# Performance work log

Hardware: AMD Instinct MI355X
Metric: run time of the kernel (lower is better)

## Reference

```python
import jax, jax.numpy as jnp
import numpy as np

THRESHOLD = 0.5
NEG_POS = 3
ALPHA = 1.0


def cxcy_to_xy(c):
    return jnp.concatenate([c[..., :2] - c[..., 2:] / 2, c[..., :2] + c[..., 2:] / 2], axis=-1)


def xy_to_cxcy(x):
    return jnp.concatenate([(x[..., :2] + x[..., 2:]) / 2, x[..., 2:] - x[..., :2]], axis=-1)


def encode_gcxgcy(cxcy, priors_cxcy):
    # SSD offset encoding with variances (10, 10, 5, 5)
    return jnp.concatenate([
        (cxcy[..., :2] - priors_cxcy[..., :2]) / (priors_cxcy[..., 2:] / 10.0),
        jnp.log(cxcy[..., 2:] / priors_cxcy[..., 2:]) * 5.0,
    ], axis=-1)


def compute_iou(a, b):
    # a: [n,4] xyxy, b: [m,4] xyxy -> [n,m]
    lt = jnp.maximum(a[:, None, :2], b[None, :, :2])
    rb = jnp.minimum(a[:, None, 2:], b[None, :, 2:])
    wh = jnp.clip(rb - lt, 0.0)
    inter = wh[..., 0] * wh[..., 1]
    area_a = (a[:, 2] - a[:, 0]) * (a[:, 3] - a[:, 1])
    area_b = (b[:, 2] - b[:, 0]) * (b[:, 3] - b[:, 1])
    return inter / (area_a[:, None] + area_b[None, :] - inter)


def _match_one(boxes, labels, db_xy, db_cxcy):
    # boxes: [n_obj,4] xyxy, labels: [n_obj], priors: [P,4]
    n_obj = boxes.shape[0]
    overlaps = compute_iou(boxes, db_xy)                 # [n_obj, P]
    ov_per_box = jnp.max(overlaps, axis=0)               # [P]
    obj_per_box = jnp.argmax(overlaps, axis=0)           # [P]
    box_per_obj = jnp.argmax(overlaps, axis=1)           # [n_obj]
    # force each gt to own its best prior
    obj_per_box = obj_per_box.at[box_per_obj].set(jnp.arange(n_obj))
    ov_per_box = ov_per_box.at[box_per_obj].set(1.0)
    lbl = labels[obj_per_box]                            # [P]
    lbl = jnp.where(ov_per_box < THRESHOLD, 0, lbl)      # background below threshold
    true_locs = encode_gcxgcy(xy_to_cxcy(boxes[obj_per_box]), db_cxcy)  # [P,4]
    return true_locs, lbl


def smooth_l1(x):
    ax = jnp.abs(x)
    return jnp.where(ax < 1.0, 0.5 * x * x, ax - 0.5)


def reference(loc_pred, cls_pred, gt_boxes, gt_labels, default_boxes):
    # loc_pred: [B,P,4], cls_pred: [B,P,C], gt_boxes: [B,n_obj,4],
    # gt_labels: [B,n_obj] int, default_boxes: [P,4] cxcywh
    db_xy = cxcy_to_xy(default_boxes)
    true_locs, true_labels = jax.vmap(_match_one, in_axes=(0, 0, None, None))(
        gt_boxes, gt_labels, db_xy, default_boxes)      # [B,P,4], [B,P]

    positive = true_labels > 0                           # [B,P]
    n_pos = jnp.sum(positive, axis=1)                    # [B]
    n_pos_total = jnp.sum(n_pos).astype(loc_pred.dtype)

    # localization loss: SmoothL1 mean over positive box elements
    loc_elem = smooth_l1(loc_pred - true_locs)           # [B,P,4]
    loc_loss = jnp.sum(loc_elem * positive[..., None]) / (n_pos_total * 4.0)

    # confidence loss: cross entropy with 3:1 hard negative mining
    logp = jax.nn.log_softmax(cls_pred, axis=-1)         # [B,P,C]
    ce = -jnp.take_along_axis(logp, true_labels[..., None], axis=-1)[..., 0]  # [B,P]
    conf_pos = jnp.sum(ce * positive)
    ce_neg = jnp.where(positive, 0.0, ce)
    # rank negatives by loss (descending) per image; take top neg_pos * n_pos
    ranks = jnp.argsort(jnp.argsort(-ce_neg, axis=1), axis=1)  # [B,P]
    hard_neg = ranks < (NEG_POS * n_pos)[:, None]
    conf_hard = jnp.sum(ce_neg * hard_neg)
    conf_loss = (conf_pos + conf_hard) / n_pos_total

    return conf_loss + ALPHA * loc_loss


def setup_inputs() -> dict:
    key = jax.random.key(0)
    ks = jax.random.split(key, 8)
    B, P, C, n_obj = 64, 8732, 81, 32

    # priors in cxcywh, valid in [0,1]
    db_cxy = jax.random.uniform(ks[0], (P, 2), minval=0.05, maxval=0.95)
    db_wh = jax.random.uniform(ks[1], (P, 2), minval=0.05, maxval=0.3)
    default_boxes = jnp.concatenate([db_cxy, db_wh], axis=-1).astype(jnp.float32)

    # gt boxes: valid xyxy built from centers and sizes
    g_cxy = jax.random.uniform(ks[2], (B, n_obj, 2), minval=0.2, maxval=0.8)
    g_wh = jax.random.uniform(ks[3], (B, n_obj, 2), minval=0.1, maxval=0.4)
    gt_boxes = jnp.concatenate([g_cxy - g_wh / 2, g_cxy + g_wh / 2], axis=-1).astype(jnp.float32)
    gt_labels = jax.random.randint(ks[4], (B, n_obj), 1, C)

    loc_pred = jax.random.normal(ks[5], (B, P, 4), dtype=jnp.float32) * 0.1
    cls_pred = jax.random.normal(ks[6], (B, P, C), dtype=jnp.float32)

    return {"loc_pred": loc_pred, "cls_pred": cls_pred, "gt_boxes": gt_boxes,
            "gt_labels": gt_labels, "default_boxes": default_boxes}
```

## Files before the change

### kernel.cpp

```cpp
#include <hip/hip_runtime.h>
#include <hip/hip_bf16.h>
#include <math.h>

#define BB 64
#define PP 8732
#define CC 81
#define NOBJ 32
#define CHUNKS ((PP + 255) / 256)
#define NPRI (BB * PP)
#define WTILE 16
#define WTW (WTILE * CC)
#define NWT (NPRI / WTILE)
#define CE_BLOCKS 1792
#define TPW 5

typedef float f4 __attribute__((ext_vector_type(4)));

__device__ __forceinline__ float sl1(float x) {
    float ax = fabsf(x);
    return (ax < 1.0f) ? 0.5f * x * x : ax - 0.5f;
}

__global__ __launch_bounds__(256) void k_bestprior(
    const float* __restrict__ gt_boxes,
    const float* __restrict__ dbox,
    int*   __restrict__ bp,
    float* __restrict__ acc,
    int*   __restrict__ npt,
    int*   __restrict__ done,
    int*   __restrict__ n_pos)
{
    __shared__ float s_bv[4];
    __shared__ int   s_bi[4];
    const int tid = threadIdx.x, lane = tid & 63, wave = tid >> 6;
    const int b = blockIdx.x >> 5;
    const int o = blockIdx.x & 31;

    if (blockIdx.x == 0) {
        if (tid < BB) n_pos[tid] = 0;
        else if (tid < BB + 3) acc[tid - BB] = 0.0f;
        else if (tid == BB + 3) *npt = 0;
        else if (tid == BB + 4) *done = 0;
    }

    const float* g = gt_boxes + (b * NOBJ + o) * 4;
    float gx0 = g[0], gy0 = g[1], gx1 = g[2], gy1 = g[3];
    float garea = (gx1 - gx0) * (gy1 - gy0);

    float best = -1.0f; int bpp = 0x7fffffff;
    for (int p = tid; p < PP; p += 256) {
        float4 db = reinterpret_cast<const float4*>(dbox)[p];
        float px0 = db.x - db.z * 0.5f, py0 = db.y - db.w * 0.5f;
        float px1 = db.x + db.z * 0.5f, py1 = db.y + db.w * 0.5f;
        float parea = db.z * db.w;
        float lx = fmaxf(px0, gx0), ly = fmaxf(py0, gy0);
        float rx = fminf(px1, gx1), ry = fminf(py1, gy1);
        float w = fmaxf(rx - lx, 0.0f), h = fmaxf(ry - ly, 0.0f);
        float inter = w * h;
        float iou = inter / (garea + parea - inter);
        if (iou > best) { best = iou; bpp = p; }
    }
#pragma unroll
    for (int m = 32; m > 0; m >>= 1) {
        float ov = __shfl_xor(best, m);
        int   op = __shfl_xor(bpp, m);
        if (ov > best || (ov == best && op < bpp)) { best = ov; bpp = op; }
    }
    if (lane == 0) { s_bv[wave] = best; s_bi[wave] = bpp; }
    __syncthreads();
    if (tid == 0) {
        for (int w2 = 1; w2 < 4; ++w2) {
            if (s_bv[w2] > best || (s_bv[w2] == best && s_bi[w2] < bpp)) {
                best = s_bv[w2]; bpp = s_bi[w2];
            }
        }
        bp[b * NOBJ + o] = bpp;
    }
}

__global__ __launch_bounds__(256) void k_assign(
    const float* __restrict__ loc_pred,
    const float* __restrict__ gt_boxes,
    const int*   __restrict__ gt_labels,
    const float* __restrict__ dbox,
    const int*   __restrict__ bp,
    int*   __restrict__ true_label,
    int*   __restrict__ n_pos,
    float* __restrict__ acc,
    int*   __restrict__ n_pos_total)
{
    __shared__ float s_gx0[NOBJ], s_gy0[NOBJ], s_gx1[NOBJ], s_gy1[NOBJ], s_garea[NOBJ];
    __shared__ float s_gcx[NOBJ], s_gcy[NOBJ], s_gw[NOBJ], s_gh[NOBJ];
    __shared__ int   s_glbl[NOBJ], s_bp[NOBJ];
    __shared__ float red_f[256];
    __shared__ int   red_i[256];

    const int b     = blockIdx.x / CHUNKS;
    const int chunk = blockIdx.x % CHUNKS;
    const int tid   = threadIdx.x;
    const int p     = chunk * 256 + tid;

    if (tid < NOBJ) {
        float x0 = gt_boxes[(b * NOBJ + tid) * 4 + 0];
        float y0 = gt_boxes[(b * NOBJ + tid) * 4 + 1];
        float x1 = gt_boxes[(b * NOBJ + tid) * 4 + 2];
        float y1 = gt_boxes[(b * NOBJ + tid) * 4 + 3];
        s_gx0[tid] = x0; s_gy0[tid] = y0; s_gx1[tid] = x1; s_gy1[tid] = y1;
        s_garea[tid] = (x1 - x0) * (y1 - y0);
        s_gcx[tid] = (x0 + x1) * 0.5f;
        s_gcy[tid] = (y0 + y1) * 0.5f;
        s_gw[tid]  = x1 - x0;
        s_gh[tid]  = y1 - y0;
        s_glbl[tid] = gt_labels[b * NOBJ + tid];
        s_bp[tid]   = bp[b * NOBJ + tid];
    }
    __syncthreads();

    float loc_local = 0.0f;
    int   np_local  = 0;

    if (p < PP) {
        float4 db = reinterpret_cast<const float4*>(dbox)[p];
        float px0 = db.x - db.z * 0.5f, py0 = db.y - db.w * 0.5f;
        float px1 = db.x + db.z * 0.5f, py1 = db.y + db.w * 0.5f;
        float parea = db.z * db.w;

        float best = -1.0f; int bo = 0;
#pragma unroll
        for (int o = 0; o < NOBJ; ++o) {
            float lx = fmaxf(px0, s_gx0[o]), ly = fmaxf(py0, s_gy0[o]);
            float rx = fminf(px1, s_gx1[o]), ry = fminf(py1, s_gy1[o]);
            float w = fmaxf(rx - lx, 0.0f), h = fmaxf(ry - ly, 0.0f);
            float inter = w * h;
            float iou = inter / (s_garea[o] + parea - inter);
            if (iou > best) { best = iou; bo = o; }
        }
        int forced = -1;
#pragma unroll
        for (int o = 0; o < NOBJ; ++o)
            if (s_bp[o] == p) forced = o;

        int o_use, lbl;
        if (forced >= 0) { o_use = forced; lbl = s_glbl[forced]; }
        else             { o_use = bo; lbl = (best < 0.5f) ? 0 : s_glbl[bo]; }

        true_label[b * PP + p] = lbl;
        if (lbl > 0) {
            np_local = 1;
            float g0 = (s_gcx[o_use] - db.x) / (db.z / 10.0f);
            float g1 = (s_gcy[o_use] - db.y) / (db.w / 10.0f);
            float g2 = logf(s_gw[o_use] / db.z) * 5.0f;
            float g3 = logf(s_gh[o_use] / db.w) * 5.0f;
            float4 lp = reinterpret_cast<const float4*>(loc_pred)[b * PP + p];
            loc_local = sl1(lp.x - g0) + sl1(lp.y - g1) + sl1(lp.z - g2) + sl1(lp.w - g3);
        }
    }

    red_f[tid] = loc_local;
    red_i[tid] = np_local;
    __syncthreads();
#pragma unroll
    for (int st = 128; st > 0; st >>= 1) {
        if (tid < st) { red_f[tid] += red_f[tid + st]; red_i[tid] += red_i[tid + st]; }
        __syncthreads();
    }
    if (tid == 0) {
        if (red_f[0] != 0.0f) atomicAdd(&acc[0], red_f[0]);
        if (red_i[0]) {
            atomicAdd(&n_pos[b], red_i[0]);
            atomicAdd(n_pos_total, red_i[0]);
        }
    }
}

__global__ __launch_bounds__(256) void k_ce(
    const float* __restrict__ cls_pred,
    const int*   __restrict__ true_label,
    float* __restrict__ ce_neg,
    float* __restrict__ acc)
{
    __shared__ float s_x[4][WTW];
    __shared__ float s_red[4];
    const int tid  = threadIdx.x;
    const int wave = tid >> 6, lane = tid & 63;
    const int rloc = lane >> 2, q = lane & 3;

    float* sx = s_x[wave];
    f4* dst = reinterpret_cast<f4*>(sx);
    const f4* tile4 = reinterpret_cast<const f4*>(sx);

    const int seg_start = rloc * CC + q * 20;
    const int seg_len   = (q == 3) ? 21 : 20;
    const int ws        = seg_start >> 2;
    const int a         = seg_start & 3;
    const int hi_cnt    = a + seg_len - 20;

    const float L2E = 1.4426950408889634f;
    const float LN2 = 0.6931471805599453f;
    float local = 0.0f;

    const int g    = blockIdx.x * 4 + wave;
    int wt         = g * TPW;
    const int wend = (wt + TPW < NWT) ? wt + TPW : NWT;

    f4 r0, r1, r2, r3, r4, r5;
    int lbl_next = 0;
    if (wt < wend) {
        const f4* src = reinterpret_cast<const f4*>(cls_pred + (size_t)wt * WTW);
        r0 = src[lane];
        r1 = src[64 + lane];
        r2 = src[128 + lane];
        r3 = src[192 + lane];
        r4 = src[256 + lane];
        if (lane < 4) r5 = src[320 + lane];
        lbl_next = true_label[wt * WTILE + rloc];
    }

    while (wt < wend) {
        dst[lane] = r0; dst[64 + lane] = r1; dst[128 + lane] = r2;
        dst[192 + lane] = r3; dst[256 + lane] = r4;
        if (lane < 4) dst[320 + lane] = r5;
        const int lbl  = lbl_next;
        const int pidx = wt * WTILE + rloc;

        const int wtn = wt + 1;
        if (wtn < wend) {
            const f4* src = reinterpret_cast<const f4*>(cls_pred + (size_t)wtn * WTW);
            r0 = src[lane];
            r1 = src[64 + lane];
            r2 = src[128 + lane];
            r3 = src[192 + lane];
            r4 = src[256 + lane];
            if (lane < 4) r5 = src[320 + lane];
            lbl_next = true_label[wtn * WTILE + rloc];
        }

        f4 w0 = tile4[ws];
        f4 w1 = tile4[ws + 1];
        f4 w2 = tile4[ws + 2];
        f4 w3 = tile4[ws + 3];
        f4 w4 = tile4[ws + 4];
        f4 w5 = tile4[ws + 5];

        float s0 = 0.0f, s1 = 0.0f;
#pragma unroll
        for (int k = 0; k < 4; ++k) {
            float e = exp2f(w0[k] * L2E);
            s0 += (k >= a) ? e : 0.0f;
        }
#pragma unroll
        for (int k = 0; k < 4; ++k) s1 += exp2f(w1[k] * L2E);
#pragma unroll
        for (int k = 0; k < 4; ++k) s0 += exp2f(w2[k] * L2E);
#pragma unroll
        for (int k = 0; k < 4; ++k) s1 += exp2f(w3[k] * L2E);
#pragma unroll
        for (int k = 0; k < 4; ++k) s0 += exp2f(w4[k] * L2E);
#pragma unroll
        for (int k = 0; k < 4; ++k) {
            float e = exp2f(w5[k] * L2E);
            s1 += (k < hi_cnt) ? e : 0.0f;
        }
        float s = s0 + s1;
        s += __shfl_xor(s, 1);
        s += __shfl_xor(s, 2);

        if (q == 0) {
            float ce = fmaf(log2f(s), LN2, -sx[rloc * CC + lbl]);
            ce_neg[pidx] = (lbl > 0) ? 0.0f : ce;
            local += (lbl > 0) ? ce : 0.0f;
        }
        wt = wtn;
    }

#pragma unroll
    for (int m = 32; m > 0; m >>= 1) local += __shfl_xor(local, m);
    if (lane == 0) s_red[wave] = local;
    __syncthreads();
    if (tid == 0) {
        float tot = s_red[0] + s_red[1] + s_red[2] + s_red[3];
        if (tot != 0.0f) atomicAdd(&acc[1], tot);
    }
}

__global__ __launch_bounds__(1024) void k_select(
    const float* __restrict__ ce_neg,
    const int*   __restrict__ n_pos,
    float* __restrict__ acc,
    const int*  __restrict__ n_pos_total,
    int*   __restrict__ done,
    float* __restrict__ out)
{
    __shared__ unsigned int sv[PP];
    __shared__ unsigned int h16[16][256];
    __shared__ unsigned int hist[257];
    __shared__ unsigned int wtot[4];
    __shared__ unsigned int s_prefix, s_krem;
    __shared__ float rf[16];
    __shared__ int   ri[16];

    const int b = blockIdx.x, tid = threadIdx.x;
    const int lane = tid & 63, w = tid >> 6;

    int K = n_pos[b] * 3;
    if (K > PP) K = PP;

    if (K > 0) {
        for (int i = tid; i < PP; i += 1024)
            sv[i] = __float_as_uint(ce_neg[b * PP + i]);

        unsigned int prefix = 0, krem = (unsigned int)K;
        for (int shift = 24; shift >= 0; shift -= 8) {
            unsigned int* hflat = &h16[0][0];
            for (int j = tid; j < 16 * 256; j += 1024) hflat[j] = 0;
            if (tid == 0) hist[256] = 0;
            __syncthreads();
            unsigned int mask_hi = (shift == 24) ? 0u : (0xFFFFFFFFu << (shift + 8));
            for (int i = tid; i < PP; i += 1024) {
                unsigned int v = sv[i];
                if ((v & mask_hi) == prefix)
                    atomicAdd(&h16[w][(v >> shift) & 0xFFu], 1u);
            }
            __syncthreads();
            unsigned int s = 0;
            if (tid < 256) {
#pragma unroll
                for (int r = 0; r < 16; ++r) s += h16[r][tid];
#pragma unroll
                for (int off = 1; off < 64; off <<= 1) {
                    unsigned int aa = __shfl_down(s, off);
                    if (lane + off < 64) s += aa;
                }
                if (lane == 0) wtot[w] = s;
            }
            __syncthreads();
            if (tid < 256) {
                unsigned int sb = 0;
#pragma unroll
                for (int r = 0; r < 16; ++r) sb += h16[r][tid];
                unsigned int suf = sb;
#pragma unroll
                for (int off = 1; off < 64; off <<= 1) {
                    unsigned int aa = __shfl_down(suf, off);
                    if (lane + off < 64) suf += aa;
                }
                for (int w2 = w + 1; w2 < 4; ++w2) suf += wtot[w2];
                hist[tid] = suf;
            }
            __syncthreads();
            if (tid < 256) {
                unsigned int suf  = hist[tid];
                unsigned int suf1 = hist[tid + 1];
                if (suf >= krem && suf1 < krem) {
                    s_prefix = prefix | ((unsigned int)tid << shift);
                    s_krem   = krem - suf1;
                }
            }
            __syncthreads();
            prefix = s_prefix; krem = s_krem;
        }
        float cutoff = __uint_as_float(prefix);

        float sum_gt = 0.0f; int cnt_gt = 0;
        for (int i = tid; i < PP; i += 1024) {
            float v = __uint_as_float(sv[i]);
            if (v > cutoff) { sum_gt += v; cnt_gt++; }
        }
#pragma unroll
        for (int m = 32; m > 0; m >>= 1) {
            sum_gt += __shfl_xor(sum_gt, m);
            cnt_gt += __shfl_xor(cnt_gt, m);
        }
        if (lane == 0) { rf[w] = sum_gt; ri[w] = cnt_gt; }
        __syncthreads();
        if (tid == 0) {
            float sg = 0.0f; int cg = 0;
#pragma unroll
            for (int r = 0; r < 16; ++r) { sg += rf[r]; cg += ri[r]; }
            atomicAdd(&acc[2], sg + (float)(K - cg) * cutoff);
        }
    }

    if (tid == 0) {
        __threadfence();
        int old = atomicAdd(done, 1);
        if (old == BB - 1) {
            float a0 = atomicAdd(&acc[0], 0.0f);
            float a1 = atomicAdd(&acc[1], 0.0f);
            float a2 = atomicAdd(&acc[2], 0.0f);
            float npt = (float)atomicAdd((int*)n_pos_total, 0);
            out[0] = (a1 + a2) / npt + a0 / (npt * 4.0f);
        }
    }
}

extern "C" void kernel_launch(void* const* d_in, const int* in_sizes, int n_in,
                              void* d_out, int out_size, void* d_ws, size_t ws_size,
                              hipStream_t stream) {
    const float* loc_pred  = (const float*)d_in[0];
    const float* cls_pred  = (const float*)d_in[1];
    const float* gt_boxes  = (const float*)d_in[2];
    const int*   gt_labels = (const int*)d_in[3];
    const float* dbox      = (const float*)d_in[4];
    float* out = (float*)d_out;

    float* acc        = (float*)d_ws;
    int*   npt        = (int*)d_ws + 3;
    int*   done       = (int*)d_ws + 4;
    int*   n_pos      = (int*)d_ws + 8;
    int*   bp         = (int*)d_ws + 8 + BB;
    int*   true_label = (int*)d_ws + 8 + BB + BB * NOBJ;
    float* ce_neg     = (float*)(true_label + (size_t)NPRI);

    k_bestprior<<<BB * NOBJ, 256, 0, stream>>>(gt_boxes, dbox, bp,
                                               acc, npt, done, n_pos);
    k_assign<<<BB * CHUNKS, 256, 0, stream>>>(loc_pred, gt_boxes, gt_labels, dbox, bp,
                                              true_label, n_pos, acc, npt);
    k_ce<<<CE_BLOCKS, 256, 0, stream>>>(cls_pred, true_label, ce_neg, acc);
    k_select<<<BB, 1024, 0, stream>>>(ce_neg, n_pos, acc, npt, done, out);
}
```

Measured before the change: 151.6 us.

## Stream CE logit tiles directly into LDS with double-buffered global_load_lds

The cross-entropy kernel now copies each 16-prior logit tile straight from global memory into LDS with global_load_lds, instead of staging it through registers and then writing it to LDS. Each wave double-buffers its tiles and uses explicit vmcnt waits to overlap the next tile's load with the current tile's reduction. All labels are prefetched up front. Blocks shrink to two waves and the grid grows to keep the same work split. The aim is to cut VGPR pressure and LDS store instructions on the bandwidth-bound logit stream, at the cost of hand-managed waitcnts that depend on how the compiler counts loads.

Result: slower. 169.8 us (+12.0%).

```diff
diff --git a/kernel.cpp b/kernel.cpp
--- a/kernel.cpp
+++ b/kernel.cpp
@@ -11,10 +11,12 @@
 #define WTILE 16
 #define WTW (WTILE * CC)
 #define NWT (NPRI / WTILE)
-#define CE_BLOCKS 1792
 #define TPW 5
+#define CE_BLOCKS 3493
 
 typedef float f4 __attribute__((ext_vector_type(4)));
+typedef const __attribute__((address_space(1))) void g_void;
+typedef __attribute__((address_space(3))) void l_void;
 
 __device__ __forceinline__ float sl1(float x) {
     float ax = fabsf(x);
@@ -173,21 +175,42 @@
     }
 }
 
-__global__ __launch_bounds__(256) void k_ce(
+#define ISSUE6(WT, LBASE)                                                         \
+    {                                                                             \
+        const char* gsrc = (const char*)(cls_pred + (size_t)(WT) * WTW);          \
+        char* lb = (char*)(LBASE);                                                \
+        __builtin_amdgcn_global_load_lds((g_void*)(gsrc + lane * 16),             \
+                                         (l_void*)(lb), 16, 0, 0);                \
+        __builtin_amdgcn_global_load_lds((g_void*)(gsrc + 1024 + lane * 16),      \
+                                         (l_void*)(lb + 1024), 16, 0, 0);         \
+        __builtin_amdgcn_global_load_lds((g_void*)(gsrc + 2048 + lane * 16),      \
+                                         (l_void*)(lb + 2048), 16, 0, 0);         \
+        __builtin_amdgcn_global_load_lds((g_void*)(gsrc + 3072 + lane * 16),      \
+                                         (l_void*)(lb + 3072), 16, 0, 0);         \
+        __builtin_amdgcn_global_load_lds((g_void*)(gsrc + 4096 + lane * 16),      \
+                                         (l_void*)(lb + 4096), 16, 0, 0);         \
+        if (lane < 4)                                                             \
+            __builtin_amdgcn_global_load_lds((g_void*)(gsrc + 5120 + lane * 16),  \
+                                             (l_void*)(lb + 5120), 16, 0, 0);     \
+    }
+
+__global__ __launch_bounds__(128) void k_ce(
     const float* __restrict__ cls_pred,
     const int*   __restrict__ true_label,
     float* __restrict__ ce_neg,
     float* __restrict__ acc)
 {
-    __shared__ float s_x[4][WTW];
-    __shared__ float s_red[4];
+    __shared__ float s_x[2][2][WTW];
+    __shared__ float s_red[2];
     const int tid  = threadIdx.x;
     const int wave = tid >> 6, lane = tid & 63;
     const int rloc = lane >> 2, q = lane & 3;
 
-    float* sx = s_x[wave];
-    f4* dst = reinterpret_cast<f4*>(sx);
-    const f4* tile4 = reinterpret_cast<const f4*>(sx);
+    const int g = blockIdx.x * 2 + wave;
+    const int wt0  = g * TPW;
+    if (wt0 >= NWT) return;
+    const int wend = (wt0 + TPW < NWT) ? wt0 + TPW : NWT;
+    const int nt   = wend - wt0;
 
     const int seg_start = rloc * CC + q * 20;
     const int seg_len   = (q == 3) ? 21 : 20;
@@ -199,41 +222,26 @@
     const float LN2 = 0.6931471805599453f;
     float local = 0.0f;
 
-    const int g    = blockIdx.x * 4 + wave;
-    int wt         = g * TPW;
-    const int wend = (wt + TPW < NWT) ? wt + TPW : NWT;
-
-    f4 r0, r1, r2, r3, r4, r5;
-    int lbl_next = 0;
-    if (wt < wend) {
-        const f4* src = reinterpret_cast<const f4*>(cls_pred + (size_t)wt * WTW);
-        r0 = src[lane];
-        r1 = src[64 + lane];
-        r2 = src[128 + lane];
-        r3 = src[192 + lane];
-        r4 = src[256 + lane];
-        if (lane < 4) r5 = src[320 + lane];
-        lbl_next = true_label[wt * WTILE + rloc];
-    }
-
-    while (wt < wend) {
-        dst[lane] = r0; dst[64 + lane] = r1; dst[128 + lane] = r2;
-        dst[192 + lane] = r3; dst[256 + lane] = r4;
-        if (lane < 4) dst[320 + lane] = r5;
-        const int lbl  = lbl_next;
-        const int pidx = wt * WTILE + rloc;
-
-        const int wtn = wt + 1;
-        if (wtn < wend) {
-            const f4* src = reinterpret_cast<const f4*>(cls_pred + (size_t)wtn * WTW);
-            r0 = src[lane];
-            r1 = src[64 + lane];
-            r2 = src[128 + lane];
-            r3 = src[192 + lane];
-            r4 = src[256 + lane];
-            if (lane < 4) r5 = src[320 + lane];
-            lbl_next = true_label[wtn * WTILE + rloc];
-        }
+    int lbls[TPW];
+#pragma unroll
+    for (int j = 0; j < TPW; ++j)
+        lbls[j] = (j < nt) ? true_label[(wt0 + j) * WTILE + rloc] : 0;
+    asm volatile("s_waitcnt vmcnt(0)" ::: "memory");
+
+    ISSUE6(wt0, s_x[wave][0]);
+
+#pragma unroll
+    for (int j = 0; j < TPW; ++j) {
+        if (j >= nt) break;
+        const int wt = wt0 + j;
+        const bool has_next = (j + 1 < nt);
+        if (has_next) ISSUE6(wt + 1, s_x[wave][(j + 1) & 1]);
+        if (has_next) asm volatile("s_waitcnt vmcnt(6)" ::: "memory");
+        else          asm volatile("s_waitcnt vmcnt(0)" ::: "memory");
+        __builtin_amdgcn_sched_barrier(0);
+
+        const float* sx = s_x[wave][j & 1];
+        const f4* tile4 = reinterpret_cast<const f4*>(sx);
 
         f4 w0 = tile4[ws];
         f4 w1 = tile4[ws + 1];
@@ -266,11 +274,12 @@
         s += __shfl_xor(s, 2);
 
         if (q == 0) {
+            const int lbl  = lbls[j];
+            const int pidx = wt * WTILE + rloc;
             float ce = fmaf(log2f(s), LN2, -sx[rloc * CC + lbl]);
             ce_neg[pidx] = (lbl > 0) ? 0.0f : ce;
             local += (lbl > 0) ? ce : 0.0f;
         }
-        wt = wtn;
     }
 
 #pragma unroll
@@ -278,7 +287,7 @@
     if (lane == 0) s_red[wave] = local;
     __syncthreads();
     if (tid == 0) {
-        float tot = s_red[0] + s_red[1] + s_red[2] + s_red[3];
+        float tot = s_red[0] + ((blockIdx.x * 2 + 1) * TPW < NWT ? s_red[1] : 0.0f);
         if (tot != 0.0f) atomicAdd(&acc[1], tot);
     }
 }
@@ -416,6 +425,6 @@
                                                acc, npt, done, n_pos);
     k_assign<<<BB * CHUNKS, 256, 0, stream>>>(loc_pred, gt_boxes, gt_labels, dbox, bp,
                                               true_label, n_pos, acc, npt);
-    k_ce<<<CE_BLOCKS, 256, 0, stream>>>(cls_pred, true_label, ce_neg, acc);
+    k_ce<<<CE_BLOCKS, 128, 0, stream>>>(cls_pred, true_label, ce_neg, acc);
     k_select<<<BB, 1024, 0, stream>>>(ce_neg, n_pos, acc, npt, done, out);
 }
```
